# Kernel optimization log

Hardware: AMD Instinct MI355X
Metric: run time of the kernel (lower is better)

The kernel has to match this reference:

```python
import jax, jax.numpy as jnp
import numpy as np

# Swin block config (matches init_kwargs)
DIM = 192
HEADS = 6
HEAD_DIM = 32
INNER = HEADS * HEAD_DIM  # 192
MLP = 768
WS = 7                    # window size
DISP = WS // 2            # cyclic shift displacement = 3
NEG = -1e9                # stands in for -inf in the shift masks
EPS = 1e-5


def setup_inputs() -> dict:
    key = jax.random.key(0)
    ks = jax.random.split(key, 8)
    B, H, W = 8, 112, 112
    x = jax.random.normal(ks[0], (B, H, W, DIM), dtype=jnp.float32)
    w_qkv = jax.random.normal(ks[1], (DIM, 3 * INNER), dtype=jnp.float32) * 0.02
    w_out = jax.random.normal(ks[2], (INNER, DIM), dtype=jnp.float32) * 0.02
    b_out = jnp.zeros((DIM,), jnp.float32)
    pos_emb = jax.random.normal(ks[3], (2 * WS - 1, 2 * WS - 1), dtype=jnp.float32)
    ln1_g = jnp.ones((DIM,), jnp.float32)
    ln1_b = jnp.zeros((DIM,), jnp.float32)
    ln2_g = jnp.ones((DIM,), jnp.float32)
    ln2_b = jnp.zeros((DIM,), jnp.float32)
    w1 = jax.random.normal(ks[4], (DIM, MLP), dtype=jnp.float32) * 0.02
    b1 = jnp.zeros((MLP,), jnp.float32)
    w2 = jax.random.normal(ks[5], (MLP, DIM), dtype=jnp.float32) * 0.02
    b2 = jnp.zeros((DIM,), jnp.float32)
    return {"x": x, "w_qkv": w_qkv, "w_out": w_out, "b_out": b_out,
            "pos_emb": pos_emb, "ln1_g": ln1_g, "ln1_b": ln1_b,
            "ln2_g": ln2_g, "ln2_b": ln2_b,
            "w1": w1, "b1": b1, "w2": w2, "b2": b2}


def _layernorm(x, g, b):
    mu = jnp.mean(x, axis=-1, keepdims=True)
    var = jnp.var(x, axis=-1, keepdims=True)
    return (x - mu) * jax.lax.rsqrt(var + EPS) * g + b


def _rel_bias(pos_emb):
    # relative position bias, gathered to (ws^2, ws^2)
    coords = jnp.stack(jnp.meshgrid(jnp.arange(WS), jnp.arange(WS), indexing="ij"), -1).reshape(-1, 2)
    rel = coords[:, None, :] - coords[None, :, :] + WS - 1  # in [0, 2*WS-2]
    return pos_emb[rel[..., 0], rel[..., 1]]


def _shift_masks(nw_h, nw_w):
    ws2 = WS * WS
    ul = jnp.zeros((ws2, ws2), jnp.float32)
    ul = ul.at[-DISP * WS:, :-DISP * WS].set(NEG)
    ul = ul.at[:-DISP * WS, -DISP * WS:].set(NEG)
    lr = jnp.zeros((WS, WS, WS, WS), jnp.float32)
    lr = lr.at[:, -DISP:, :, :-DISP].set(NEG)
    lr = lr.at[:, :-DISP:, :, -DISP:].set(NEG)
    lr = lr.reshape(ws2, ws2)
    full = jnp.zeros((nw_h * nw_w, ws2, ws2), jnp.float32)
    full = full.at[-nw_w:].add(ul)            # bottom row of windows
    full = full.at[nw_w - 1::nw_w].add(lr)    # rightmost column of windows
    return full


def _window_attention(x, w_qkv, w_out, b_out, pos_emb):
    x = jnp.roll(x, (-DISP, -DISP), axis=(1, 2))  # cyclic shift
    B, H, W, _ = x.shape
    nw_h, nw_w = H // WS, W // WS
    ws2 = WS * WS
    qkv = x @ w_qkv  # (B,H,W,3*INNER)
    qkv = qkv.reshape(B, nw_h, WS, nw_w, WS, 3, HEADS, HEAD_DIM)
    # -> (3, B, heads, n_windows, ws^2, head_dim)
    qkv = qkv.transpose(5, 0, 6, 1, 3, 2, 4, 7).reshape(3, B, HEADS, nw_h * nw_w, ws2, HEAD_DIM)
    q, k, v = qkv[0], qkv[1], qkv[2]
    dots = jnp.einsum("bhwid,bhwjd->bhwij", q, k) * (HEAD_DIM ** -0.5)
    dots = dots + _rel_bias(pos_emb)                       # (ws2,ws2) broadcast
    dots = dots + _shift_masks(nw_h, nw_w)                 # (nw,ws2,ws2) broadcast
    attn = jax.nn.softmax(dots, axis=-1)
    out = jnp.einsum("bhwij,bhwjd->bhwid", attn, v)
    # merge windows back: (B, nw_h, WS, nw_w, WS, heads*head_dim)
    out = out.reshape(B, HEADS, nw_h, nw_w, WS, WS, HEAD_DIM)
    out = out.transpose(0, 2, 4, 3, 5, 1, 6).reshape(B, H, W, INNER)
    out = out @ w_out + b_out
    return jnp.roll(out, (DISP, DISP), axis=(1, 2))  # cyclic back-shift


def reference(x, w_qkv, w_out, b_out, pos_emb, ln1_g, ln1_b, ln2_g, ln2_b, w1, b1, w2, b2):
    # Residual(PreNorm(WindowAttention))
    x = x + _window_attention(_layernorm(x, ln1_g, ln1_b), w_qkv, w_out, b_out, pos_emb)
    # Residual(PreNorm(FeedForward))  with exact (erf) GELU as in nn.GELU
    h = _layernorm(x, ln2_g, ln2_b)
    h = jax.nn.gelu(h @ w1 + b1, approximate=False) @ w2 + b2
    return x + h
```

## Files before the change

### kernel.cpp

```cpp
#include <hip/hip_runtime.h>
#include <hip/hip_bf16.h>
#include <math.h>

typedef __hip_bfloat16 bf16;
typedef unsigned short ushort_t;
typedef __bf16 bf16x8 __attribute__((ext_vector_type(8)));
typedef unsigned short ushortx8 __attribute__((ext_vector_type(8)));
typedef float  f32x4  __attribute__((ext_vector_type(4)));

#define BATCH 8
#define HH 112
#define WW 112
#define CDIM 192
#define HEADS 6
#define HD 32
#define QKVW 576
#define MLPW 768
#define WS 7
#define WS2 49
#define NWH 16
#define NWW 16
#define NWIN 256
#define NTOK (BATCH*HH*WW)
#define NEGV (-1e9f)

typedef __attribute__((address_space(3))) void lds_void;
typedef const __attribute__((address_space(1))) void gbl_void;

__device__ __forceinline__ float toF(float v) { return v; }
__device__ __forceinline__ float toF(bf16 v) { return __bfloat162float(v); }
__device__ __forceinline__ bf16  f2b(float v) { return __float2bfloat16(v); }
__device__ __forceinline__ ushort_t f2u(float v) { bf16 b = __float2bfloat16(v); return *(ushort_t*)&b; }

__device__ __forceinline__ bool probe_is_bf16(const void* p) {
    const unsigned int* w = (const unsigned int*)p;
    int nz = 0, band = 0;
    #pragma unroll
    for (int i = 0; i < 16; i++) {
        unsigned int v = w[i];
        if (v == 0u) continue;
        nz++;
        unsigned int lo = v & 0xFFFFu, hi = v >> 16;
        unsigned int elo = (lo >> 7) & 0xFFu, ehi = (hi >> 7) & 0xFFu;
        bool okl = (lo != 0u) && (elo >= 0x60u) && (elo <= 0x9Fu);
        bool okh = (hi != 0u) && (ehi >= 0x60u) && (ehi <= 0x9Fu);
        if (okl && okh) band++;
    }
    return (nz == 0) || (band == nz);
}

__device__ __forceinline__ float read_any(const void* p, size_t i, bool isb) {
    return isb ? toF(((const bf16*)p)[i]) : ((const float*)p)[i];
}

__device__ __forceinline__ float wave_sum(float v) {
    #pragma unroll
    for (int o = 1; o < 64; o <<= 1) v += __shfl_xor(v, o, 64);
    return v;
}

__global__ void canon_kernel(const void* __restrict__ src, float* __restrict__ dst, int n) {
    bool isb = probe_is_bf16(src);
    int i = blockIdx.x * 256 + threadIdx.x;
    if (i < n) dst[i] = read_any(src, i, isb);
}

__global__ void canon_bt_kernel(const void* __restrict__ src, ushort_t* __restrict__ dstT,
                                int K, int N) {
    bool isb = probe_is_bf16(src);
    int i = blockIdx.x * 256 + threadIdx.x;
    if (i < K * N) {
        int k = i / N, n = i % N;
        dstT[(size_t)n * K + k] = f2u(read_any(src, i, isb));
    }
}

__global__ void ln1_kernel(const void* __restrict__ xraw, const float* __restrict__ g,
                           const float* __restrict__ bta, bf16* __restrict__ out) {
    bool xb = probe_is_bf16(xraw);
    int wave = threadIdx.x >> 6, lane = threadIdx.x & 63;
    int t = blockIdx.x * 4 + wave;
    size_t base = (size_t)t * CDIM;
    float v[3];
    #pragma unroll
    for (int i = 0; i < 3; i++) v[i] = read_any(xraw, base + lane + 64 * i, xb);
    float s  = v[0] + v[1] + v[2];
    float s2 = v[0]*v[0] + v[1]*v[1] + v[2]*v[2];
    s = wave_sum(s); s2 = wave_sum(s2);
    float mu = s * (1.0f / CDIM);
    float var = s2 * (1.0f / CDIM) - mu * mu;
    float rs = rsqrtf(var + 1e-5f);
    #pragma unroll
    for (int i = 0; i < 3; i++) {
        int c = lane + 64 * i;
        out[base + c] = f2b((v[i] - mu) * rs * g[c] + bta[c]);
    }
}

template <int EPI, int NY>
__global__ __launch_bounds__(256) void gemm_kernel(
    const ushort_t* __restrict__ A, const ushort_t* __restrict__ BT,
    const int K, const int N,
    const float* __restrict__ bias,
    const void* __restrict__ res,
    void* __restrict__ out)
{
    __shared__ ushort_t As[2][128 * 64];
    __shared__ ushort_t Bs[2][64 * 64];
    int tid = threadIdx.x;
    int per = gridDim.x >> 3;
    int sid = blockIdx.x;
    int w = (sid & 7) * per + (sid >> 3);
    int t0 = (w / NY) * 128;
    int n0 = (w % NY) * 64;
    int lane = tid & 63, wv = tid >> 6;
    int l15 = lane & 15, quad = lane >> 4;
    int lr = lane >> 3;
    int lc = lane & 7;

    f32x4 acc[2][4];
    #pragma unroll
    for (int i = 0; i < 2; i++)
        #pragma unroll
        for (int j = 0; j < 4; j++)
            acc[i][j] = (f32x4){0.f, 0.f, 0.f, 0.f};

    auto stage = [&](int kb, int buf) {
        #pragma unroll
        for (int it = 0; it < 4; it++) {
            int r = wv * 32 + it * 8 + lr;
            const ushort_t* src = &A[(size_t)(t0 + r) * K + kb + ((lc ^ (r & 7)) << 3)];
            __builtin_amdgcn_global_load_lds(
                (gbl_void*)src, (lds_void*)&As[buf][(wv * 32 + it * 8) * 64], 16, 0, 0);
        }
        #pragma unroll
        for (int it = 0; it < 2; it++) {
            int r = wv * 16 + it * 8 + lr;
            const ushort_t* src = &BT[(size_t)(n0 + r) * K + kb + ((lc ^ (r & 7)) << 3)];
            __builtin_amdgcn_global_load_lds(
                (gbl_void*)src, (lds_void*)&Bs[buf][(wv * 16 + it * 8) * 64], 16, 0, 0);
        }
    };

    const int nkb = K >> 6;
    stage(0, 0);
    __syncthreads();

    for (int t = 0; t < nkb; t++) {
        int cur = t & 1;
        if (t + 1 < nkb) stage((t + 1) << 6, cur ^ 1);
        #pragma unroll
        for (int kk = 0; kk < 64; kk += 32) {
            int cs = (((kk >> 3) + quad) ^ (l15 & 7)) << 3;
            bf16x8 af[2], bfr[4];
            #pragma unroll
            for (int i = 0; i < 2; i++)
                af[i] = *(const bf16x8*)(&As[cur][(wv * 32 + i * 16 + l15) * 64 + cs]);
            #pragma unroll
            for (int j = 0; j < 4; j++)
                bfr[j] = *(const bf16x8*)(&Bs[cur][(j * 16 + l15) * 64 + cs]);
            #pragma unroll
            for (int i = 0; i < 2; i++)
                #pragma unroll
                for (int j = 0; j < 4; j++)
                    acc[i][j] = __builtin_amdgcn_mfma_f32_16x16x32_bf16(af[i], bfr[j], acc[i][j], 0, 0, 0);
        }
        __syncthreads();
    }

    bool xb = false;
    if (EPI == 1) xb = probe_is_bf16(res);

    #pragma unroll
    for (int i = 0; i < 2; i++) {
        #pragma unroll
        for (int j = 0; j < 4; j++) {
            #pragma unroll
            for (int r = 0; r < 4; r++) {
                int row = wv * 32 + i * 16 + quad * 4 + r;
                int col = n0 + j * 16 + l15;
                size_t t = (size_t)(t0 + row);
                float v = acc[i][j][r];
                if (EPI == 0) {
                    ((bf16*)out)[t * N + col] = f2b(v);
                } else {
                    size_t o = t * CDIM + col;
                    ((bf16*)out)[o] = f2b(v + bias[col] + read_any(res, o, xb));
                }
            }
        }
    }
}

__global__ __launch_bounds__(256) void fused_mlp_kernel(
    const bf16* __restrict__ X,
    const ushort_t* __restrict__ W1T,
    const ushort_t* __restrict__ W2T,
    const float* __restrict__ g, const float* __restrict__ bta,
    const float* __restrict__ b1, const float* __restrict__ b2,
    float* __restrict__ out)
{
    __shared__ ushort_t W1s[3 * 64 * 64];
    __shared__ ushort_t W2s[192 * 64];
    __shared__ ushort_t Hs[64 * 64];
    int tid = threadIdx.x;
    int lane = tid & 63, wv = tid >> 6;
    int l15 = lane & 15, quad = lane >> 4;
    int lr = lane >> 3, lc = lane & 7;
    int t0 = blockIdx.x * 64;

    size_t rb = (size_t)(t0 + wv * 16 + l15) * CDIM;
    float va[6][8];
    float s = 0.f, s2 = 0.f;
    #pragma unroll
    for (int kk = 0; kk < 6; kk++) {
        bf16x8 v = *(const bf16x8*)((const ushort_t*)X + rb + kk * 32 + quad * 8);
        #pragma unroll
        for (int j = 0; j < 8; j++) {
            float f = (float)v[j];
            va[kk][j] = f; s += f; s2 += f * f;
        }
    }
    s  += __shfl_xor(s, 16, 64);  s  += __shfl_xor(s, 32, 64);
    s2 += __shfl_xor(s2, 16, 64); s2 += __shfl_xor(s2, 32, 64);
    float mu = s * (1.0f / CDIM);
    float var = s2 * (1.0f / CDIM) - mu * mu;
    float rs = rsqrtf(var + 1e-5f);
    bf16x8 af[6];
    #pragma unroll
    for (int kk = 0; kk < 6; kk++) {
        int c0 = kk * 32 + quad * 8;
        float4 g0 = *(const float4*)(g + c0), g1 = *(const float4*)(g + c0 + 4);
        float4 b0 = *(const float4*)(bta + c0), b1v = *(const float4*)(bta + c0 + 4);
        const float* gp[2] = {&g0.x, &g1.x};
        const float* bp[2] = {&b0.x, &b1v.x};
        #pragma unroll
        for (int j = 0; j < 8; j++)
            af[kk][j] = (__bf16)((va[kk][j] - mu) * rs * gp[j >> 2][j & 3] + bp[j >> 2][j & 3]);
    }

    f32x4 acc2[12];
    #pragma unroll
    for (int nt = 0; nt < 12; nt++) acc2[nt] = (f32x4){0.f, 0.f, 0.f, 0.f};

    for (int c = 0; c < 12; c++) {
        #pragma unroll
        for (int rg = 0; rg < 2; rg++) {
            int rowb = wv * 16 + rg * 8;
            #pragma unroll
            for (int p = 0; p < 3; p++) {
                const ushort_t* src =
                    &W1T[(size_t)(c * 64 + rowb + lr) * CDIM + p * 64 + ((lc ^ lr) << 3)];
                __builtin_amdgcn_global_load_lds(
                    (gbl_void*)src, (lds_void*)&W1s[p * 4096 + rowb * 64], 16, 0, 0);
            }
        }
        #pragma unroll
        for (int rg = 0; rg < 6; rg++) {
            int rowb = wv * 48 + rg * 8;
            const ushort_t* src =
                &W2T[(size_t)(rowb + lr) * MLPW + c * 64 + ((lc ^ lr) << 3)];
            __builtin_amdgcn_global_load_lds(
                (gbl_void*)src, (lds_void*)&W2s[rowb * 64], 16, 0, 0);
        }
        __syncthreads();

        f32x4 hacc[4];
        #pragma unroll
        for (int nt = 0; nt < 4; nt++) hacc[nt] = (f32x4){0.f, 0.f, 0.f, 0.f};
        #pragma unroll
        for (int kk = 0; kk < 6; kk++) {
            int p = kk >> 1;
            int cc = (kk & 1) * 4 + quad;
            #pragma unroll
            for (int nt = 0; nt < 4; nt++) {
                int n = nt * 16 + l15;
                bf16x8 bfr = *(const bf16x8*)(&W1s[p * 4096 + n * 64 + ((cc ^ (n & 7)) << 3)]);
                hacc[nt] = __builtin_amdgcn_mfma_f32_16x16x32_bf16(af[kk], bfr, hacc[nt], 0, 0, 0);
            }
        }
        #pragma unroll
        for (int nt = 0; nt < 4; nt++) {
            #pragma unroll
            for (int r = 0; r < 4; r++) {
                int i = wv * 16 + quad * 4 + r;
                int hcol = nt * 16 + l15;
                float a = hacc[nt][r] + b1[c * 64 + hcol];
                float gl = 0.5f * a * (1.0f + erff(a * 0.70710678118654752f));
                Hs[i * 64 + (((hcol >> 3) ^ (i & 7)) << 3) + (hcol & 7)] = f2u(gl);
            }
        }
        __syncthreads();

        #pragma unroll
        for (int kt = 0; kt < 2; kt++) {
            int row = wv * 16 + l15;
            int cc = kt * 4 + quad;
            bf16x8 pa = *(const bf16x8*)(&Hs[row * 64 + ((cc ^ (row & 7)) << 3)]);
            #pragma unroll
            for (int nt = 0; nt < 12; nt++) {
                int n = nt * 16 + l15;
                bf16x8 wb = *(const bf16x8*)(&W2s[n * 64 + ((cc ^ (n & 7)) << 3)]);
                acc2[nt] = __builtin_amdgcn_mfma_f32_16x16x32_bf16(pa, wb, acc2[nt], 0, 0, 0);
            }
        }
        __syncthreads();
    }

    #pragma unroll
    for (int nt = 0; nt < 12; nt++) {
        #pragma unroll
        for (int r = 0; r < 4; r++) {
            int row = t0 + wv * 16 + quad * 4 + r;
            int col = nt * 16 + l15;
            size_t o = (size_t)row * CDIM + col;
            out[o] = acc2[nt][r] + b2[col] + toF(X[o]);
        }
    }
}

__global__ __launch_bounds__(256) void attn_kernel(const bf16* __restrict__ qkv,
                                                   const float* __restrict__ pos_emb,
                                                   bf16* __restrict__ y) {
    __shared__ ushort_t Ps[4][64 * 72];
    __shared__ ushort_t Vt[4][32 * 72];
    __shared__ float pe[169];

    int tid = threadIdx.x;
    int wv = tid >> 6, lane = tid & 63;
    int l15 = lane & 15, quad = lane >> 4;

    int per = gridDim.x >> 3;
    int sid = blockIdx.x;
    int bid = (sid & 7) * per + (sid >> 3);
    int gid = bid * 4 + wv;
    int h = gid % HEADS;
    int rest = gid / HEADS;
    int win = rest % NWIN;
    int b = rest / NWIN;
    int wi = win >> 4, wj = win & 15;

    for (int i = lane; i < 169; i += 64) pe[i] = pos_emb[i];
    __syncthreads();

    auto tok = [&](int i) -> int {
        i = min(i, 48);
        int pi = (i * 37) >> 8;
        int pj = i - pi * 7;
        int ui = wi * WS + pi + 3; if (ui >= HH) ui -= HH;
        int uj = wj * WS + pj + 3; if (uj >= WW) uj -= WW;
        return (b * HH + ui) * WW + uj;
    };

    bf16x8 qf[4], kf[4];
    #pragma unroll
    for (int t = 0; t < 4; t++) {
        size_t base = (size_t)tok(t * 16 + l15) * QKVW + h * HD + quad * 8;
        qf[t] = *(const bf16x8*)(qkv + base);
        kf[t] = *(const bf16x8*)(qkv + base + CDIM);
    }

    #pragma unroll
    for (int it = 0; it < 4; it++) {
        int idx = lane + it * 64;
        int p = idx >> 2, dc = idx & 3;
        size_t base = (size_t)tok(p) * QKVW + 2 * CDIM + h * HD + dc * 8;
        ushortx8 v = *(const ushortx8*)((const ushort_t*)qkv + base);
        #pragma unroll
        for (int jj = 0; jj < 8; jj++)
            Vt[wv][(dc * 8 + jj) * 72 + p] = v[jj];
    }

    f32x4 acc[4][4];
    #pragma unroll
    for (int mt = 0; mt < 4; mt++)
        #pragma unroll
        for (int nt = 0; nt < 4; nt++)
            acc[mt][nt] = (f32x4){0.f, 0.f, 0.f, 0.f};
    #pragma unroll
    for (int mt = 0; mt < 4; mt++)
        #pragma unroll
        for (int nt = 0; nt < 4; nt++)
            acc[mt][nt] = __builtin_amdgcn_mfma_f32_16x16x32_bf16(qf[mt], kf[nt], acc[mt][nt], 0, 0, 0);

    bool m_ul = (wi == NWH - 1);
    bool m_lr = (wj == NWW - 1);
    int kpi[4], kpj[4];
    bool jval[4];
    #pragma unroll
    for (int nt = 0; nt < 4; nt++) {
        int j = nt * 16 + l15;
        jval[nt] = (j < WS2);
        int jc = min(j, 48);
        kpi[nt] = (jc * 37) >> 8;
        kpj[nt] = jc - kpi[nt] * 7;
    }
    #pragma unroll
    for (int mt = 0; mt < 4; mt++) {
        #pragma unroll
        for (int r = 0; r < 4; r++) {
            int i = mt * 16 + quad * 4 + r;
            int ic = min(i, 48);
            int pi = (ic * 37) >> 8;
            int pj = ic - pi * 7;
            #pragma unroll
            for (int nt = 0; nt < 4; nt++) {
                float s = acc[mt][nt][r] * 0.17677669529663689f
                        + pe[(pi - kpi[nt] + 6) * 13 + (pj - kpj[nt] + 6)];
                if (m_ul && ((pi >= 4) != (kpi[nt] >= 4))) s += NEGV;
                if (m_lr && ((pj >= 4) != (kpj[nt] >= 4))) s += NEGV;
                if (!jval[nt]) s = NEGV;
                acc[mt][nt][r] = s;
            }
            float mx = fmaxf(fmaxf(acc[mt][0][r], acc[mt][1][r]),
                             fmaxf(acc[mt][2][r], acc[mt][3][r]));
            #pragma unroll
            for (int o = 1; o < 16; o <<= 1) mx = fmaxf(mx, __shfl_xor(mx, o, 64));
            float sum = 0.f;
            #pragma unroll
            for (int nt = 0; nt < 4; nt++) {
                float e = __expf(acc[mt][nt][r] - mx);
                acc[mt][nt][r] = e;
                sum += e;
            }
            #pragma unroll
            for (int o = 1; o < 16; o <<= 1) sum += __shfl_xor(sum, o, 64);
            float inv = 1.0f / sum;
            #pragma unroll
            for (int nt = 0; nt < 4; nt++) acc[mt][nt][r] *= inv;
        }
    }

    #pragma unroll
    for (int mt = 0; mt < 4; mt++)
        #pragma unroll
        for (int nt = 0; nt < 4; nt++)
            #pragma unroll
            for (int r = 0; r < 4; r++)
                Ps[wv][(mt * 16 + quad * 4 + r) * 72 + nt * 16 + l15] = f2u(acc[mt][nt][r]);

    f32x4 oacc[4][2];
    #pragma unroll
    for (int mt = 0; mt < 4; mt++)
        #pragma unroll
        for (int nt = 0; nt < 2; nt++)
            oacc[mt][nt] = (f32x4){0.f, 0.f, 0.f, 0.f};
    #pragma unroll
    for (int kt = 0; kt < 2; kt++) {
        bf16x8 pa[4], vb[2];
        #pragma unroll
        for (int mt = 0; mt < 4; mt++)
            pa[mt] = *(const bf16x8*)(&Ps[wv][(mt * 16 + l15) * 72 + kt * 32 + quad * 8]);
        #pragma unroll
        for (int nt = 0; nt < 2; nt++)
            vb[nt] = *(const bf16x8*)(&Vt[wv][(nt * 16 + l15) * 72 + kt * 32 + quad * 8]);
        #pragma unroll
        for (int mt = 0; mt < 4; mt++)
            #pragma unroll
            for (int nt = 0; nt < 2; nt++)
                oacc[mt][nt] = __builtin_amdgcn_mfma_f32_16x16x32_bf16(pa[mt], vb[nt], oacc[mt][nt], 0, 0, 0);
    }

    #pragma unroll
    for (int mt = 0; mt < 4; mt++) {
        #pragma unroll
        for (int r = 0; r < 4; r++) {
            int i = mt * 16 + quad * 4 + r;
            if (i < WS2) {
                size_t base = (size_t)tok(i) * CDIM + h * HD + l15;
                #pragma unroll
                for (int nt = 0; nt < 2; nt++)
                    y[base + nt * 16] = f2b(oacc[mt][nt][r]);
            }
        }
    }
}

extern "C" void kernel_launch(void* const* d_in, const int* in_sizes, int n_in,
                              void* d_out, int out_size, void* d_ws, size_t ws_size,
                              hipStream_t stream) {
    float* out = (float*)d_out;

    size_t szA = (size_t)NTOK * CDIM * sizeof(bf16);
    size_t szQ = (size_t)NTOK * QKVW * sizeof(bf16);
    size_t szY = (size_t)NTOK * CDIM * sizeof(bf16);
    size_t szX = (size_t)NTOK * CDIM * sizeof(bf16);
    size_t szP = 3072 * sizeof(float);
    size_t szT = 442368 * sizeof(ushort_t);
    if (ws_size < szA + szQ + szY + szX + szP + szT) return;
    bf16*     bufA = (bf16*)d_ws;
    bf16*     bufQ = (bf16*)((char*)d_ws + szA);
    bf16*     bufY = (bf16*)((char*)d_ws + szA + szQ);
    bf16*     bufX = (bf16*)((char*)d_ws + szA + szQ + szY);
    float*    cW   = (float*)((char*)d_ws + szA + szQ + szY + szX);
    ushort_t* cT   = (ushort_t*)((char*)d_ws + szA + szQ + szY + szX + szP);

    float* cBout = cW + 0;
    float* cPe   = cW + 192;
    float* cL1g  = cW + 384;
    float* cL1b  = cW + 576;
    float* cL2g  = cW + 768;
    float* cL2b  = cW + 960;
    float* cB1   = cW + 1152;
    float* cB2   = cW + 1920;

    ushort_t* tWqkv = cT + 0;
    ushort_t* tWout = cT + 110592;
    ushort_t* tW1   = cT + 147456;
    ushort_t* tW2   = cT + 294912;

    dim3 b256(256);
    #define CANON(src, dst, n) canon_kernel<<<((n)+255)/256, b256, 0, stream>>>((src), (dst), (n))
    CANON(d_in[3],  cBout, 192);
    CANON(d_in[4],  cPe,   169);
    CANON(d_in[5],  cL1g,  192);
    CANON(d_in[6],  cL1b,  192);
    CANON(d_in[7],  cL2g,  192);
    CANON(d_in[8],  cL2b,  192);
    CANON(d_in[10], cB1,   768);
    CANON(d_in[12], cB2,   192);
    #undef CANON
    #define CANONT(src, dst, K, N) \
        canon_bt_kernel<<<((K)*(N)+255)/256, b256, 0, stream>>>((src), (dst), (K), (N))
    CANONT(d_in[1],  tWqkv, CDIM, QKVW);
    CANONT(d_in[2],  tWout, CDIM, CDIM);
    CANONT(d_in[9],  tW1,   CDIM, MLPW);
    CANONT(d_in[11], tW2,   MLPW, CDIM);
    #undef CANONT

    int gLN = NTOK / 4;
    int gM  = NTOK / 128;
    int gAT = BATCH * NWIN * HEADS / 4;
    int gF  = NTOK / 64;

    ln1_kernel<<<gLN, b256, 0, stream>>>(d_in[0], cL1g, cL1b, bufA);
    gemm_kernel<0, 9><<<gM * 9, b256, 0, stream>>>(
        (const ushort_t*)bufA, tWqkv, CDIM, QKVW, nullptr, nullptr, bufQ);
    attn_kernel<<<gAT, b256, 0, stream>>>(bufQ, cPe, bufY);
    gemm_kernel<1, 3><<<gM * 3, b256, 0, stream>>>(
        (const ushort_t*)bufY, tWout, CDIM, CDIM, cBout, d_in[0], bufX);
    fused_mlp_kernel<<<gF, b256, 0, stream>>>(
        bufX, tW1, tW2, cL2g, cL2b, cB1, cB2, out);
}
```

Measured before the change: 546.5 us.

## Double MLP row tile to 128 and prefetch next weight chunk

The fused MLP kernel now processes 128 tokens per block (two 16-row sub-tiles per wave), so each staged W1/W2 chunk in LDS feeds twice as many MFMAs and total weight traffic halves. Weight staging for the next chunk is issued right after the barrier that frees each buffer, overlapping the global-to-LDS copy with the current compute instead of stalling at the top of each iteration. Doubling accumulators raises register pressure (launch bounds now ask for 2 blocks per CU), and the grid halves, which may reduce occupancy and parallelism.

Result: no change. 536.2 us (-1.9%).

```diff
diff --git a/kernel.cpp b/kernel.cpp
--- a/kernel.cpp
+++ b/kernel.cpp
@@ -192,7 +192,7 @@
     }
 }
 
-__global__ __launch_bounds__(256) void fused_mlp_kernel(
+__global__ __launch_bounds__(256, 2) void fused_mlp_kernel(
     const bf16* __restrict__ X,
     const ushort_t* __restrict__ W1T,
     const ushort_t* __restrict__ W2T,
@@ -202,31 +202,59 @@
 {
     __shared__ ushort_t W1s[3 * 64 * 64];
     __shared__ ushort_t W2s[192 * 64];
-    __shared__ ushort_t Hs[64 * 64];
+    __shared__ ushort_t Hs[128 * 64];
     int tid = threadIdx.x;
     int lane = tid & 63, wv = tid >> 6;
     int l15 = lane & 15, quad = lane >> 4;
     int lr = lane >> 3, lc = lane & 7;
-    int t0 = blockIdx.x * 64;
-
-    size_t rb = (size_t)(t0 + wv * 16 + l15) * CDIM;
-    float va[6][8];
-    float s = 0.f, s2 = 0.f;
-    #pragma unroll
-    for (int kk = 0; kk < 6; kk++) {
-        bf16x8 v = *(const bf16x8*)((const ushort_t*)X + rb + kk * 32 + quad * 8);
-        #pragma unroll
-        for (int j = 0; j < 8; j++) {
-            float f = (float)v[j];
-            va[kk][j] = f; s += f; s2 += f * f;
-        }
-    }
-    s  += __shfl_xor(s, 16, 64);  s  += __shfl_xor(s, 32, 64);
-    s2 += __shfl_xor(s2, 16, 64); s2 += __shfl_xor(s2, 32, 64);
-    float mu = s * (1.0f / CDIM);
-    float var = s2 * (1.0f / CDIM) - mu * mu;
-    float rs = rsqrtf(var + 1e-5f);
-    bf16x8 af[6];
+    int t0 = blockIdx.x * 128;
+
+    auto stageW1 = [&](int c) {
+        #pragma unroll
+        for (int p = 0; p < 3; p++)
+            #pragma unroll
+            for (int rg = 0; rg < 2; rg++) {
+                int rowb = wv * 16 + rg * 8;
+                const ushort_t* src =
+                    &W1T[(size_t)(c * 64 + rowb + lr) * CDIM + p * 64 + ((lc ^ lr) << 3)];
+                __builtin_amdgcn_global_load_lds(
+                    (gbl_void*)src, (lds_void*)&W1s[p * 4096 + rowb * 64], 16, 0, 0);
+            }
+    };
+    auto stageW2 = [&](int c) {
+        #pragma unroll
+        for (int rg = 0; rg < 6; rg++) {
+            int rowb = wv * 48 + rg * 8;
+            const ushort_t* src =
+                &W2T[(size_t)(rowb + lr) * MLPW + c * 64 + ((lc ^ lr) << 3)];
+            __builtin_amdgcn_global_load_lds(
+                (gbl_void*)src, (lds_void*)&W2s[rowb * 64], 16, 0, 0);
+        }
+    };
+
+    stageW1(0);
+    stageW2(0);
+
+    bf16x8 af[2][6];
+    float s[2] = {0.f, 0.f}, s2[2] = {0.f, 0.f};
+    #pragma unroll
+    for (int m = 0; m < 2; m++) {
+        size_t rb = (size_t)(t0 + wv * 32 + m * 16 + l15) * CDIM;
+        #pragma unroll
+        for (int kk = 0; kk < 6; kk++) {
+            af[m][kk] = *(const bf16x8*)((const ushort_t*)X + rb + kk * 32 + quad * 8);
+            #pragma unroll
+            for (int j = 0; j < 8; j++) {
+                float f = (float)af[m][kk][j];
+                s[m] += f; s2[m] += f * f;
+            }
+        }
+    }
+    #pragma unroll
+    for (int m = 0; m < 2; m++) {
+        s[m]  += __shfl_xor(s[m], 16, 64);  s[m]  += __shfl_xor(s[m], 32, 64);
+        s2[m] += __shfl_xor(s2[m], 16, 64); s2[m] += __shfl_xor(s2[m], 32, 64);
+    }
     #pragma unroll
     for (int kk = 0; kk < 6; kk++) {
         int c0 = kk * 32 + quad * 8;
@@ -235,39 +263,31 @@
         const float* gp[2] = {&g0.x, &g1.x};
         const float* bp[2] = {&b0.x, &b1v.x};
         #pragma unroll
-        for (int j = 0; j < 8; j++)
-            af[kk][j] = (__bf16)((va[kk][j] - mu) * rs * gp[j >> 2][j & 3] + bp[j >> 2][j & 3]);
-    }
-
-    f32x4 acc2[12];
-    #pragma unroll
-    for (int nt = 0; nt < 12; nt++) acc2[nt] = (f32x4){0.f, 0.f, 0.f, 0.f};
+        for (int m = 0; m < 2; m++) {
+            float mu = s[m] * (1.0f / CDIM);
+            float var = s2[m] * (1.0f / CDIM) - mu * mu;
+            float rs = rsqrtf(var + 1e-5f);
+            #pragma unroll
+            for (int j = 0; j < 8; j++)
+                af[m][kk][j] = (__bf16)(((float)af[m][kk][j] - mu) * rs * gp[j >> 2][j & 3]
+                                        + bp[j >> 2][j & 3]);
+        }
+    }
+
+    f32x4 acc2[2][12];
+    #pragma unroll
+    for (int m = 0; m < 2; m++)
+        #pragma unroll
+        for (int nt = 0; nt < 12; nt++) acc2[m][nt] = (f32x4){0.f, 0.f, 0.f, 0.f};
+
+    __syncthreads();
 
     for (int c = 0; c < 12; c++) {
-        #pragma unroll
-        for (int rg = 0; rg < 2; rg++) {
-            int rowb = wv * 16 + rg * 8;
-            #pragma unroll
-            for (int p = 0; p < 3; p++) {
-                const ushort_t* src =
-                    &W1T[(size_t)(c * 64 + rowb + lr) * CDIM + p * 64 + ((lc ^ lr) << 3)];
-                __builtin_amdgcn_global_load_lds(
-                    (gbl_void*)src, (lds_void*)&W1s[p * 4096 + rowb * 64], 16, 0, 0);
-            }
-        }
-        #pragma unroll
-        for (int rg = 0; rg < 6; rg++) {
-            int rowb = wv * 48 + rg * 8;
-            const ushort_t* src =
-                &W2T[(size_t)(rowb + lr) * MLPW + c * 64 + ((lc ^ lr) << 3)];
-            __builtin_amdgcn_global_load_lds(
-                (gbl_void*)src, (lds_void*)&W2s[rowb * 64], 16, 0, 0);
-        }
-        __syncthreads();
-
-        f32x4 hacc[4];
-        #pragma unroll
-        for (int nt = 0; nt < 4; nt++) hacc[nt] = (f32x4){0.f, 0.f, 0.f, 0.f};
+        f32x4 hacc[2][4];
+        #pragma unroll
+        for (int m = 0; m < 2; m++)
+            #pragma unroll
+            for (int nt = 0; nt < 4; nt++) hacc[m][nt] = (f32x4){0.f, 0.f, 0.f, 0.f};
         #pragma unroll
         for (int kk = 0; kk < 6; kk++) {
             int p = kk >> 1;
@@ -276,45 +296,67 @@
             for (int nt = 0; nt < 4; nt++) {
                 int n = nt * 16 + l15;
                 bf16x8 bfr = *(const bf16x8*)(&W1s[p * 4096 + n * 64 + ((cc ^ (n & 7)) << 3)]);
-                hacc[nt] = __builtin_amdgcn_mfma_f32_16x16x32_bf16(af[kk], bfr, hacc[nt], 0, 0, 0);
-            }
-        }
-        #pragma unroll
-        for (int nt = 0; nt < 4; nt++) {
-            #pragma unroll
-            for (int r = 0; r < 4; r++) {
-                int i = wv * 16 + quad * 4 + r;
-                int hcol = nt * 16 + l15;
-                float a = hacc[nt][r] + b1[c * 64 + hcol];
-                float gl = 0.5f * a * (1.0f + erff(a * 0.70710678118654752f));
-                Hs[i * 64 + (((hcol >> 3) ^ (i & 7)) << 3) + (hcol & 7)] = f2u(gl);
+                #pragma unroll
+                for (int m = 0; m < 2; m++)
+                    hacc[m][nt] = __builtin_amdgcn_mfma_f32_16x16x32_bf16(af[m][kk], bfr, hacc[m][nt], 0, 0, 0);
+            }
+        }
+        float b1v[4];
+        #pragma unroll
+        for (int nt = 0; nt < 4; nt++) b1v[nt] = b1[c * 64 + nt * 16 + l15];
+        #pragma unroll
+        for (int m = 0; m < 2; m++) {
+            #pragma unroll
+            for (int nt = 0; nt < 4; nt++) {
+                #pragma unroll
+                for (int r = 0; r < 4; r++) {
+                    int i = wv * 32 + m * 16 + quad * 4 + r;
+                    int hcol = nt * 16 + l15;
+                    float a = hacc[m][nt][r] + b1v[nt];
+                    float gl = 0.5f * a * (1.0f + erff(a * 0.70710678118654752f));
+                    Hs[i * 64 + (((hcol >> 3) ^ (i & 7)) << 3) + (hcol & 7)] = f2u(gl);
+                }
             }
         }
         __syncthreads();
 
+        if (c + 1 < 12) stageW1(c + 1);
+
         #pragma unroll
         for (int kt = 0; kt < 2; kt++) {
-            int row = wv * 16 + l15;
             int cc = kt * 4 + quad;
-            bf16x8 pa = *(const bf16x8*)(&Hs[row * 64 + ((cc ^ (row & 7)) << 3)]);
+            bf16x8 pa[2];
+            #pragma unroll
+            for (int m = 0; m < 2; m++) {
+                int row = wv * 32 + m * 16 + l15;
+                pa[m] = *(const bf16x8*)(&Hs[row * 64 + ((cc ^ (row & 7)) << 3)]);
+            }
             #pragma unroll
             for (int nt = 0; nt < 12; nt++) {
                 int n = nt * 16 + l15;
                 bf16x8 wb = *(const bf16x8*)(&W2s[n * 64 + ((cc ^ (n & 7)) << 3)]);
-                acc2[nt] = __builtin_amdgcn_mfma_f32_16x16x32_bf16(pa, wb, acc2[nt], 0, 0, 0);
+                #pragma unroll
+                for (int m = 0; m < 2; m++)
+                    acc2[m][nt] = __builtin_amdgcn_mfma_f32_16x16x32_bf16(pa[m], wb, acc2[m][nt], 0, 0, 0);
             }
         }
         __syncthreads();
+
+        if (c + 1 < 12) stageW2(c + 1);
     }
 
     #pragma unroll
     for (int nt = 0; nt < 12; nt++) {
-        #pragma unroll
-        for (int r = 0; r < 4; r++) {
-            int row = t0 + wv * 16 + quad * 4 + r;
-            int col = nt * 16 + l15;
-            size_t o = (size_t)row * CDIM + col;
-            out[o] = acc2[nt][r] + b2[col] + toF(X[o]);
+        float bb = b2[nt * 16 + l15];
+        #pragma unroll
+        for (int m = 0; m < 2; m++) {
+            #pragma unroll
+            for (int r = 0; r < 4; r++) {
+                int row = t0 + wv * 32 + m * 16 + quad * 4 + r;
+                int col = nt * 16 + l15;
+                size_t o = (size_t)row * CDIM + col;
+                out[o] = acc2[m][nt][r] + bb + toF(X[o]);
+            }
         }
     }
 }
@@ -531,7 +573,7 @@
     int gLN = NTOK / 4;
     int gM  = NTOK / 128;
     int gAT = BATCH * NWIN * HEADS / 4;
-    int gF  = NTOK / 64;
+    int gF  = NTOK / 128;
 
     ln1_kernel<<<gLN, b256, 0, stream>>>(d_in[0], cL1g, cL1b, bufA);
     gemm_kernel<0, 9><<<gM * 9, b256, 0, stream>>>(
```
